# Kernel tuning notes

Hardware: AMD Instinct MI355X
Metric: run time of the kernel (lower is better)

The kernel has to match this reference:

```python
import jax, jax.numpy as jnp
import numpy as np

N, E, D = 50000, 200000, 128   # graph nodes, graph edges (= line-graph nodes), feature dim
L = 2                          # number of GINEConv iterations (linegraph init arg)


def _build_line_graph(col0, col1):
    """Exact sparse equivalent of torch.nonzero((col1[:,None]==col0[None,:]) & (col0[:,None]!=col1[:,None])).
    Returns line edges (i -> j) with col1[i] == col0[j] and edge i not a self-loop,
    plus edge_attr_idx = col1[lg_src] (the shared graph node)."""
    order = np.argsort(col0, kind='stable')              # edges grouped by source node
    counts = np.bincount(col0, minlength=N)              # out-degree per node
    offsets = np.concatenate([[0], np.cumsum(counts)[:-1]])
    lengths = np.where(col0 != col1, counts[col1], 0)    # successors of each non-self-loop edge
    M = int(lengths.sum())
    lg_src = np.repeat(np.arange(E), lengths)
    cum = np.cumsum(lengths)
    pos = np.arange(M) - np.repeat(cum - lengths, lengths)  # position within each successor block
    lg_dst = order[np.repeat(offsets[col1], lengths) + pos]
    edge_attr_idx = col1[lg_src]
    return lg_src.astype(np.int64), lg_dst.astype(np.int64), edge_attr_idx.astype(np.int64)


def setup_inputs() -> dict:
    rng = np.random.RandomState(0)
    col0 = rng.randint(0, N, size=E).astype(np.int64)
    col1 = rng.randint(0, N, size=E).astype(np.int64)
    lg_src, lg_dst, edge_attr_idx = _build_line_graph(col0, col1)

    key = jax.random.key(0)
    kx, k1, k2 = jax.random.split(key, 3)
    scale = (2.0 / D) ** 0.5
    return {
        'x':  jax.random.normal(kx, (N, D), dtype=jnp.float32),
        'W1': jax.random.normal(k1, (D, D), dtype=jnp.float32) * scale,
        'b1': jnp.zeros((D,), dtype=jnp.float32),
        'W2': jax.random.normal(k2, (D, D), dtype=jnp.float32) * scale,
        'b2': jnp.zeros((D,), dtype=jnp.float32),
        'col0': jnp.asarray(col0),
        'col1': jnp.asarray(col1),
        'lg_src': jnp.asarray(lg_src),
        'lg_dst': jnp.asarray(lg_dst),
        'edge_attr_idx': jnp.asarray(edge_attr_idx),
    }


def reference(x, W1, b1, W2, b2, col0, col1, lg_src, lg_dst, edge_attr_idx):
    # line-graph node features: mean of endpoint features of each original edge
    lgX = 0.5 * (x[col0] + x[col1])                       # [E, D]
    lgE = x[edge_attr_idx]                                # [M, D] line-edge attrs (fixed across iterations)

    for _ in range(L):  # GINEConv, eps = 0 (PyG default)
        m = jax.nn.relu(lgX[lg_src] + lgE)                # [M, D] messages
        aggr = jax.ops.segment_sum(m, lg_dst, num_segments=E)  # scatter-add at target line-nodes
        h = lgX + aggr                                    # (1 + eps) * x + aggr
        lgX = jax.nn.relu(h @ W1 + b1) @ W2 + b2          # gin_nn MLP

    # scatter_mean back to graph nodes by col1 (zeros where no incident edge, matching pad)
    sums = jax.ops.segment_sum(lgX, col1, num_segments=N)                     # [N, D]
    cnt = jax.ops.segment_sum(jnp.ones((lgX.shape[0], 1), lgX.dtype), col1, num_segments=N)
    gx = jnp.where(cnt > 0, sums / jnp.maximum(cnt, 1.0), 0.0)

    out = jax.nn.relu(gx)
    # dropout p=0.0 -> identity; residual=True
    return x + out
```

## Files before the change

kernel.cpp:

```cpp
#include <hip/hip_runtime.h>
#include <hip/hip_bf16.h>

constexpr int NN = 50000;
constexpr int EE = 200000;
typedef __bf16 bf16x8 __attribute__((ext_vector_type(8)));
typedef float f32x4 __attribute__((ext_vector_type(4)));

__device__ __forceinline__ float b2f(unsigned short s) {
    union { unsigned u; float f; } c; c.u = ((unsigned)s) << 16; return c.f;
}
__device__ __forceinline__ unsigned short bfbits(float f) {
    union { __bf16 b; unsigned short u; } c; c.b = (__bf16)f; return c.u;
}
__device__ __forceinline__ unsigned pkbf(float lo, float hi) {
    return ((unsigned)bfbits(hi) << 16) | bfbits(lo);
}
__device__ __forceinline__ unsigned short f2b(float f) {
    union { float f; unsigned u; } c; c.f = f;
    unsigned u = c.u + 0x7fffu + ((c.u >> 16) & 1u);
    return (unsigned short)(u >> 16);
}
__device__ __forceinline__ float xv(const void* p, long i, int f32m) {
    return f32m ? ((const float*)p)[i] : b2f(((const unsigned short*)p)[i]);
}
__device__ __forceinline__ int iv(const int* p, int i, int i64m) {
    return i64m ? p[2 * i] : p[i];
}

__global__ void k_detect(const unsigned short* x16, const int* c32, int* flg) {
    __shared__ int sf, si;
    int t = threadIdx.x;
    if (t == 0) { sf = 0; si = 1; }
    __syncthreads();
    for (int i = t; i < 16384; i += 256)
        if (((x16[i] >> 7) & 0xFF) == 0xFF) sf = 1;
    if (t < 64)
        if (c32[2 * t + 1] != 0) si = 0;
    __syncthreads();
    if (t == 0) { flg[0] = sf; flg[1] = si; }
}

__global__ void k_cast(const void* x, unsigned short* xb, const int* flg) {
    int i = blockIdx.x * 256 + threadIdx.x;
    if (i >= NN * 16) return;
    if (flg[0]) {
        const float4* xp = (const float4*)x + (size_t)i * 2;
        float4 u = xp[0], v = xp[1];
        uint4 o;
        o.x = pkbf(u.x, u.y); o.y = pkbf(u.z, u.w);
        o.z = pkbf(v.x, v.y); o.w = pkbf(v.z, v.w);
        ((uint4*)xb)[i] = o;
    } else {
        ((uint4*)xb)[i] = ((const uint4*)x)[i];
    }
}

__global__ void k_wfrag2(const void* W1, const void* W2,
                         unsigned short* Wf1, unsigned short* Wf2, const int* flg) {
    int f32m = flg[0];
    int g = blockIdx.x;
    const void* W = (g < 8) ? W1 : W2;
    unsigned short* Wf = (g < 8) ? Wf1 : Wf2;
    int chunk = (g & 7) * 256 + threadIdx.x;
    int l = chunk & 63, c = (chunk >> 6) & 3, t = chunk >> 8;
    int n = t * 16 + (l & 15), k0 = c * 32 + ((l >> 4) * 8);
    for (int j = 0; j < 8; j++) Wf[chunk * 8 + j] = bfbits(xv(W, (long)(k0 + j) * 128 + n, f32m));
}

__global__ void k_hist(const int* col1, int* counts, const int* flg) {
    int e = blockIdx.x * 256 + threadIdx.x;
    if (e >= EE) return;
    atomicAdd(&counts[iv(col1, e, flg[1])], 1);
}

__global__ void k_scan1(const int* counts, int* bsum) {
    __shared__ int sh[256];
    int b = blockIdx.x, t = threadIdx.x;
    int idx = b * 256 + t;
    sh[t] = (idx < NN) ? counts[idx] : 0;
    __syncthreads();
    for (int off = 128; off > 0; off >>= 1) {
        if (t < off) sh[t] += sh[t + off];
        __syncthreads();
    }
    if (t == 0) bsum[b] = sh[0];
}

__global__ void k_scan2(const int* counts, const int* bsum,
                        int* row_ptr, int* cursor) {
    __shared__ int sh[256];
    __shared__ int base_s;
    int b = blockIdx.x, t = threadIdx.x;
    sh[t] = (t < b) ? bsum[t] : 0;
    __syncthreads();
    for (int off = 128; off > 0; off >>= 1) {
        if (t < off) sh[t] += sh[t + off];
        __syncthreads();
    }
    if (t == 0) base_s = sh[0];
    __syncthreads();
    int idx = b * 256 + t;
    int v = (idx < NN) ? counts[idx] : 0;
    sh[t] = v;
    __syncthreads();
    for (int off = 1; off < 256; off <<= 1) {
        int add = (t >= off) ? sh[t - off] : 0;
        __syncthreads();
        sh[t] += add;
        __syncthreads();
    }
    int ex = base_s + sh[t] - v;
    if (idx < NN) { row_ptr[idx] = ex; cursor[idx] = ex; }
    if (idx == NN - 1) row_ptr[NN] = ex + v;
}

__global__ void k_cscatter(const int* col0, const int* col1, int* cursor,
                           unsigned* aux, int* node1, const int* flg) {
    int e = blockIdx.x * 256 + threadIdx.x;
    if (e >= EE) return;
    int i64m = flg[1];
    int a = iv(col0, e, i64m), b = iv(col1, e, i64m);
    int pos = atomicAdd(&cursor[b], 1);
    aux[pos] = (unsigned)a | (a == b ? 0x80000000u : 0u);
    node1[pos] = b;
}

__global__ void k_gath(const unsigned short* xb, const unsigned short* lgX,
                       const int* row_ptr, const unsigned* aux,
                       unsigned short* S, int mode) {
    int n = blockIdx.x * 4 + (threadIdx.x >> 6);
    if (n >= NN) return;
    int l = threadIdx.x & 63, k0 = l * 2;
    int lo = row_ptr[n], hi = row_ptr[n + 1];
    unsigned un = *(const unsigned*)(xb + (size_t)n * 128 + k0);
    float xn0 = b2f((unsigned short)un), xn1 = b2f((unsigned short)(un >> 16));
    float a0 = 0.0f, a1 = 0.0f;
    if (mode == 1) {
        for (int p = lo; p < hi; p++) {
            unsigned av = aux[p];
            if (av & 0x80000000u) continue;
            unsigned u = *(const unsigned*)(xb + (size_t)av * 128 + k0);
            a0 += fmaxf(0.5f * b2f((unsigned short)u) + 1.5f * xn0, 0.0f);
            a1 += fmaxf(0.5f * b2f((unsigned short)(u >> 16)) + 1.5f * xn1, 0.0f);
        }
    } else {
        for (int p = lo; p < hi; p++) {
            if (aux[p] & 0x80000000u) continue;
            unsigned u = *(const unsigned*)(lgX + (size_t)p * 128 + k0);
            a0 += fmaxf(b2f((unsigned short)u) + xn0, 0.0f);
            a1 += fmaxf(b2f((unsigned short)(u >> 16)) + xn1, 0.0f);
        }
    }
    *(unsigned*)(S + (size_t)n * 128 + k0) = pkbf(a0, a1);
}

__global__ __launch_bounds__(256, 8)
void k_fused(const unsigned short* A, const unsigned short* S,
             const unsigned* aux, const int* node1, const unsigned short* xb,
             const void* bias1, const void* bias2,
             const unsigned short* Wf1, const unsigned short* Wf2,
             unsigned short* Out, const int* flg, int initA) {
    __shared__ unsigned short Lds[8192];
    int f32m = flg[0];
    int tid = threadIdx.x;
    int w = tid >> 6, l = tid & 63;
    int lq = l >> 4, ln = l & 15;
    int e0 = blockIdx.x * 64 + w * 16;
    unsigned short* W_ = Lds + w * 2048;

    int row = e0 + ln;
    int aN = (int)(aux[row] & 0x7fffffffu);
    int bN = initA ? node1[row] : 0;
    bf16x8 af[4];
    for (int c = 0; c < 4; c++) {
        int k0 = c * 32 + lq * 8;
        uint4 svv = *(const uint4*)(S + (size_t)aN * 128 + k0);
        const unsigned short* sp = (const unsigned short*)&svv;
        if (initA) {
            uint4 xav = *(const uint4*)(xb + (size_t)aN * 128 + k0);
            uint4 xbv = *(const uint4*)(xb + (size_t)bN * 128 + k0);
            const unsigned short* xa = (const unsigned short*)&xav;
            const unsigned short* xc = (const unsigned short*)&xbv;
            for (int j = 0; j < 8; j++)
                af[c][j] = (__bf16)(0.5f * (b2f(xa[j]) + b2f(xc[j])) + b2f(sp[j]));
        } else {
            uint4 av = *(const uint4*)(A + (size_t)row * 128 + k0);
            const unsigned short* ap = (const unsigned short*)&av;
            for (int j = 0; j < 8; j++)
                af[c][j] = (__bf16)(b2f(ap[j]) + b2f(sp[j]));
        }
    }

    f32x4 acc[8];
    for (int j = 0; j < 8; j++)
        for (int r = 0; r < 4; r++) acc[j][r] = 0.0f;
    for (int c = 0; c < 4; c++) {
        for (int j = 0; j < 8; j++) {
            bf16x8 bf = *(const bf16x8*)(Wf1 + (size_t)(((j * 4 + c) * 64 + l) * 8));
            acc[j] = __builtin_amdgcn_mfma_f32_16x16x32_bf16(af[c], bf, acc[j], 0, 0, 0);
        }
    }

    for (int j = 0; j < 8; j++) {
        int n = j * 16 + ln;
        float bv = xv(bias1, n, f32m);
        int c2 = n >> 5, lhi = ((n >> 3) & 3) * 16, j2 = n & 7;
        for (int rg = 0; rg < 4; rg++) {
            float h = fmaxf(acc[j][rg] + bv, 0.0f);
            W_[(c2 * 64 + lhi + lq * 4 + rg) * 8 + j2] = bfbits(h);
        }
    }

    for (int j = 0; j < 8; j++)
        for (int r = 0; r < 4; r++) acc[j][r] = 0.0f;
    for (int c = 0; c < 4; c++) {
        bf16x8 a2 = *(const bf16x8*)(W_ + (c * 64 + l) * 8);
        for (int j = 0; j < 8; j++) {
            bf16x8 bf = *(const bf16x8*)(Wf2 + (size_t)(((j * 4 + c) * 64 + l) * 8));
            acc[j] = __builtin_amdgcn_mfma_f32_16x16x32_bf16(a2, bf, acc[j], 0, 0, 0);
        }
    }

    for (int j = 0; j < 8; j++) {
        int n = j * 16 + ln;
        float bv = xv(bias2, n, f32m);
        for (int rg = 0; rg < 4; rg++)
            W_[(lq * 4 + rg) * 128 + n] = bfbits(acc[j][rg] + bv);
    }
    for (int i = 0; i < 4; i++) {
        int idx = i * 64 + l;
        ((uint4*)Out)[(size_t)e0 * 16 + idx] = ((const uint4*)W_)[idx];
    }
}

__global__ void LGNNGINELayer_12463995093126_kernel(
    const void* x, const unsigned short* lgX, const int* row_ptr,
    void* out, const int* flg) {
    int n = blockIdx.x * 4 + (threadIdx.x >> 6);
    if (n >= NN) return;
    int l = threadIdx.x & 63, k0 = l * 2;
    int f32m = flg[0];
    int lo = row_ptr[n], hi = row_ptr[n + 1];
    float a0 = 0.0f, a1 = 0.0f;
    for (int p = lo; p < hi; p++) {
        unsigned u = *(const unsigned*)(lgX + (size_t)p * 128 + k0);
        a0 += b2f((unsigned short)u);
        a1 += b2f((unsigned short)(u >> 16));
    }
    float g0 = 0.0f, g1 = 0.0f;
    if (hi > lo) {
        float inv = 1.0f / (float)(hi - lo);
        g0 = fmaxf(a0 * inv, 0.0f);
        g1 = fmaxf(a1 * inv, 0.0f);
    }
    if (f32m) {
        ((float*)out)[(long)n * 128 + k0]     = ((const float*)x)[(long)n * 128 + k0] + g0;
        ((float*)out)[(long)n * 128 + k0 + 1] = ((const float*)x)[(long)n * 128 + k0 + 1] + g1;
    } else {
        unsigned u = *(const unsigned*)((const unsigned short*)x + (long)n * 128 + k0);
        float r0 = b2f((unsigned short)u) + g0;
        float r1 = b2f((unsigned short)(u >> 16)) + g1;
        *(unsigned*)((unsigned short*)out + (long)n * 128 + k0) = pkbf(r0, r1);
    }
}

extern "C" void kernel_launch(void* const* d_in, const int* in_sizes, int n_in,
                              void* d_out, int out_size, void* d_ws, size_t ws_size,
                              hipStream_t stream) {
    (void)in_sizes; (void)n_in; (void)out_size; (void)ws_size;
    const void* x = d_in[0];
    const void* W1 = d_in[1];
    const void* b1 = d_in[2];
    const void* W2 = d_in[3];
    const void* b2 = d_in[4];
    const int* col0 = (const int*)d_in[5];
    const int* col1 = (const int*)d_in[6];

    char* p = (char*)d_ws;
    unsigned short* lgX = (unsigned short*)p; p += (size_t)EE * 128 * 2;
    unsigned short* S = (unsigned short*)p;   p += (size_t)NN * 128 * 2;
    unsigned short* xb = (unsigned short*)p;  p += (size_t)NN * 128 * 2;
    int* row_ptr = (int*)p;                   p += (size_t)(NN + 16) * 4;
    int* cursor = (int*)p;                    p += (size_t)NN * 4;
    int* counts = (int*)p;                    p += (size_t)NN * 4;
    int* bsum = (int*)p;                      p += 256 * 4;
    unsigned* aux = (unsigned*)p;             p += (size_t)EE * 4;
    int* node1 = (int*)p;                     p += (size_t)EE * 4;
    int* flg = (int*)p;                       p += 256;
    unsigned short* Wf1 = (unsigned short*)p; p += 16384 * 2;
    unsigned short* Wf2 = (unsigned short*)p;

    int gB = EE / 64;
    int eB = (EE + 255) / 256;
    int nB4 = (NN + 3) / 4;
    int sB = (NN + 255) / 256;
    int cB = (NN * 16 + 255) / 256;

    k_detect<<<1, 256, 0, stream>>>((const unsigned short*)x, col0, flg);
    k_cast<<<cB, 256, 0, stream>>>(x, xb, flg);
    k_wfrag2<<<16, 256, 0, stream>>>(W1, W2, Wf1, Wf2, flg);

    hipMemsetAsync(counts, 0, (size_t)NN * 4, stream);
    k_hist<<<eB, 256, 0, stream>>>(col1, counts, flg);
    k_scan1<<<sB, 256, 0, stream>>>(counts, bsum);
    k_scan2<<<sB, 256, 0, stream>>>(counts, bsum, row_ptr, cursor);
    k_cscatter<<<eB, 256, 0, stream>>>(col0, col1, cursor, aux, node1, flg);

    k_gath<<<nB4, 256, 0, stream>>>(xb, lgX, row_ptr, aux, S, 1);
    k_fused<<<gB, 256, 0, stream>>>(lgX, S, aux, node1, xb, b1, b2,
                                    Wf1, Wf2, lgX, flg, 1);
    k_gath<<<nB4, 256, 0, stream>>>(xb, lgX, row_ptr, aux, S, 2);
    k_fused<<<gB, 256, 0, stream>>>(lgX, S, aux, node1, xb, b1, b2,
                                    Wf1, Wf2, lgX, flg, 0);
    LGNNGINELayer_12463995093126_kernel<<<nB4, 256, 0, stream>>>(
        x, lgX, row_ptr, d_out, flg);
}
```

Before: 385.2 us.

## Fuse final scatter-mean segment sums into second GIN MLP kernel epilogue

The second fused MLP kernel no longer writes its bf16 line-node features back to global memory. Instead it reduces its 64 sorted rows by destination node inside the block and writes fp32 partial sums into a node-sum buffer, using atomics only for segments that cross block boundaries. The final kernel becomes a simple elementwise divide-by-degree, relu and residual add. This removes the lgX write and re-read for the last layer, at the cost of an extra 25.6MB memset, fp32 atomics, and a serial 64-row loop run by one wave per block.

After: 400.0 us. +3.8%, slower.

```diff
diff --git a/kernel.cpp b/kernel.cpp
--- a/kernel.cpp
+++ b/kernel.cpp
@@ -14,11 +14,6 @@
 }
 __device__ __forceinline__ unsigned pkbf(float lo, float hi) {
     return ((unsigned)bfbits(hi) << 16) | bfbits(lo);
-}
-__device__ __forceinline__ unsigned short f2b(float f) {
-    union { float f; unsigned u; } c; c.f = f;
-    unsigned u = c.u + 0x7fffu + ((c.u >> 16) & 1u);
-    return (unsigned short)(u >> 16);
 }
 __device__ __forceinline__ float xv(const void* p, long i, int f32m) {
     return f32m ? ((const float*)p)[i] : b2f(((const unsigned short*)p)[i]);
@@ -159,24 +154,26 @@
              const unsigned* aux, const int* node1, const unsigned short* xb,
              const void* bias1, const void* bias2,
              const unsigned short* Wf1, const unsigned short* Wf2,
-             unsigned short* Out, const int* flg, int initA) {
+             unsigned short* Out, float* NS, const int* flg, int mode) {
     __shared__ unsigned short Lds[8192];
+    __shared__ int nd[66];
     int f32m = flg[0];
     int tid = threadIdx.x;
     int w = tid >> 6, l = tid & 63;
     int lq = l >> 4, ln = l & 15;
-    int e0 = blockIdx.x * 64 + w * 16;
+    int eb = blockIdx.x * 64;
+    int e0 = eb + w * 16;
     unsigned short* W_ = Lds + w * 2048;
 
     int row = e0 + ln;
     int aN = (int)(aux[row] & 0x7fffffffu);
-    int bN = initA ? node1[row] : 0;
+    int bN = (mode == 1) ? node1[row] : 0;
     bf16x8 af[4];
     for (int c = 0; c < 4; c++) {
         int k0 = c * 32 + lq * 8;
         uint4 svv = *(const uint4*)(S + (size_t)aN * 128 + k0);
         const unsigned short* sp = (const unsigned short*)&svv;
-        if (initA) {
+        if (mode == 1) {
             uint4 xav = *(const uint4*)(xb + (size_t)aN * 128 + k0);
             uint4 xbv = *(const uint4*)(xb + (size_t)bN * 128 + k0);
             const unsigned short* xa = (const unsigned short*)&xav;
@@ -227,41 +224,55 @@
         for (int rg = 0; rg < 4; rg++)
             W_[(lq * 4 + rg) * 128 + n] = bfbits(acc[j][rg] + bv);
     }
-    for (int i = 0; i < 4; i++) {
-        int idx = i * 64 + l;
-        ((uint4*)Out)[(size_t)e0 * 16 + idx] = ((const uint4*)W_)[idx];
+
+    if (mode == 1) {
+        for (int i = 0; i < 4; i++) {
+            int idx = i * 64 + l;
+            ((uint4*)Out)[(size_t)e0 * 16 + idx] = ((const uint4*)W_)[idx];
+        }
+        return;
+    }
+
+    if (tid < 64) nd[tid] = node1[eb + tid];
+    else if (tid == 64) nd[64] = (eb > 0) ? node1[eb - 1] : -1;
+    else if (tid == 65) nd[65] = (eb + 64 < EE) ? node1[eb + 64] : -1;
+    __syncthreads();
+    if (tid < 64) {
+        int c2 = tid * 2;
+        float a0 = 0.0f, a1 = 0.0f;
+        int cur = nd[0];
+        bool openL = (nd[64] == cur);
+        for (int r = 0; r < 64; r++) {
+            unsigned v = *(const unsigned*)(Lds + ((r >> 4) * 2048 + (r & 15) * 128 + c2));
+            a0 += b2f((unsigned short)v);
+            a1 += b2f((unsigned short)(v >> 16));
+            bool last = (r == 63);
+            int nxt = last ? nd[65] : nd[r + 1];
+            if (nxt != cur || last) {
+                bool closedR = (nxt != cur);
+                float* dst = NS + (size_t)cur * 128 + c2;
+                if (!openL && closedR) { dst[0] = a0; dst[1] = a1; }
+                else { atomicAdd(&dst[0], a0); atomicAdd(&dst[1], a1); }
+                a0 = 0.0f; a1 = 0.0f;
+                cur = nxt;
+                openL = false;
+            }
+        }
     }
 }
 
 __global__ void LGNNGINELayer_12463995093126_kernel(
-    const void* x, const unsigned short* lgX, const int* row_ptr,
+    const void* x, const float* NS, const int* row_ptr,
     void* out, const int* flg) {
-    int n = blockIdx.x * 4 + (threadIdx.x >> 6);
-    if (n >= NN) return;
-    int l = threadIdx.x & 63, k0 = l * 2;
-    int f32m = flg[0];
-    int lo = row_ptr[n], hi = row_ptr[n + 1];
-    float a0 = 0.0f, a1 = 0.0f;
-    for (int p = lo; p < hi; p++) {
-        unsigned u = *(const unsigned*)(lgX + (size_t)p * 128 + k0);
-        a0 += b2f((unsigned short)u);
-        a1 += b2f((unsigned short)(u >> 16));
-    }
-    float g0 = 0.0f, g1 = 0.0f;
-    if (hi > lo) {
-        float inv = 1.0f / (float)(hi - lo);
-        g0 = fmaxf(a0 * inv, 0.0f);
-        g1 = fmaxf(a1 * inv, 0.0f);
-    }
-    if (f32m) {
-        ((float*)out)[(long)n * 128 + k0]     = ((const float*)x)[(long)n * 128 + k0] + g0;
-        ((float*)out)[(long)n * 128 + k0 + 1] = ((const float*)x)[(long)n * 128 + k0 + 1] + g1;
-    } else {
-        unsigned u = *(const unsigned*)((const unsigned short*)x + (long)n * 128 + k0);
-        float r0 = b2f((unsigned short)u) + g0;
-        float r1 = b2f((unsigned short)(u >> 16)) + g1;
-        *(unsigned*)((unsigned short*)out + (long)n * 128 + k0) = pkbf(r0, r1);
-    }
+    int i = blockIdx.x * 256 + threadIdx.x;
+    if (i >= NN * 128) return;
+    int n = i >> 7;
+    int deg = row_ptr[n + 1] - row_ptr[n];
+    float g = 0.0f;
+    if (deg > 0) g = fmaxf(NS[i] / (float)deg, 0.0f);
+    float r = xv(x, i, flg[0]) + g;
+    if (flg[0]) ((float*)out)[i] = r;
+    else ((unsigned short*)out)[i] = bfbits(r);
 }
 
 extern "C" void kernel_launch(void* const* d_in, const int* in_sizes, int n_in,
@@ -280,6 +291,7 @@
     unsigned short* lgX = (unsigned short*)p; p += (size_t)EE * 128 * 2;
     unsigned short* S = (unsigned short*)p;   p += (size_t)NN * 128 * 2;
     unsigned short* xb = (unsigned short*)p;  p += (size_t)NN * 128 * 2;
+    float* NS = (float*)p;                    p += (size_t)NN * 128 * 4;
     int* row_ptr = (int*)p;                   p += (size_t)(NN + 16) * 4;
     int* cursor = (int*)p;                    p += (size_t)NN * 4;
     int* counts = (int*)p;                    p += (size_t)NN * 4;
@@ -293,6 +305,7 @@
     int gB = EE / 64;
     int eB = (EE + 255) / 256;
     int nB4 = (NN + 3) / 4;
+    int nBe = (NN * 128) / 256;
     int sB = (NN + 255) / 256;
     int cB = (NN * 16 + 255) / 256;
 
@@ -308,10 +321,11 @@
 
     k_gath<<<nB4, 256, 0, stream>>>(xb, lgX, row_ptr, aux, S, 1);
     k_fused<<<gB, 256, 0, stream>>>(lgX, S, aux, node1, xb, b1, b2,
-                                    Wf1, Wf2, lgX, flg, 1);
+                                    Wf1, Wf2, lgX, NS, flg, 1);
     k_gath<<<nB4, 256, 0, stream>>>(xb, lgX, row_ptr, aux, S, 2);
+    hipMemsetAsync(NS, 0, (size_t)NN * 128 * 4, stream);
     k_fused<<<gB, 256, 0, stream>>>(lgX, S, aux, node1, xb, b1, b2,
-                                    Wf1, Wf2, lgX, flg, 0);
-    LGNNGINELayer_12463995093126_kernel<<<nB4, 256, 0, stream>>>(
-        x, lgX, row_ptr, d_out, flg);
-}
+                                    Wf1, Wf2, lgX, NS, flg, 2);
+    LGNNGINELayer_12463995093126_kernel<<<nBe, 256, 0, stream>>>(
+        x, NS, row_ptr, d_out, flg);
+}
```

## Keep line-graph features in two orderings to make fused gathers coalesced

Applied to the files above, without the earlier changes.

Builds a second CSR ordering by col0 next to the col1 ordering. The fused MLP kernel now processes edges in col0 order, so the node-level sums T are gathered per source node. Results are written both sequentially (col0 copy, used as the residual input) and scattered into col1 order for the gather and final kernels. The initial lgX term is folded into the node sum in k_gath, which drops the x[col0] read in the first MLP. Setup kernels are merged and counts are doubled to cover both orderings. The cost is an extra E×D output buffer with scattered 16-byte row writes, plus extra atomics and index arrays.

Measured after the change: 395.2 us. 2.6% more time.

```diff
diff --git a/kernel.cpp b/kernel.cpp
--- a/kernel.cpp
+++ b/kernel.cpp
@@ -3,6 +3,8 @@
 
 constexpr int NN = 50000;
 constexpr int EE = 200000;
+constexpr int SB = (NN + 255) / 256;
+constexpr int CB = (NN * 16 + 255) / 256;
 typedef __bf16 bf16x8 __attribute__((ext_vector_type(8)));
 typedef float f32x4 __attribute__((ext_vector_type(4)));
 
@@ -14,11 +16,6 @@
 }
 __device__ __forceinline__ unsigned pkbf(float lo, float hi) {
     return ((unsigned)bfbits(hi) << 16) | bfbits(lo);
-}
-__device__ __forceinline__ unsigned short f2b(float f) {
-    union { float f; unsigned u; } c; c.f = f;
-    unsigned u = c.u + 0x7fffu + ((c.u >> 16) & 1u);
-    return (unsigned short)(u >> 16);
 }
 __device__ __forceinline__ float xv(const void* p, long i, int f32m) {
     return f32m ? ((const float*)p)[i] : b2f(((const unsigned short*)p)[i]);
@@ -40,44 +37,50 @@
     if (t == 0) { flg[0] = sf; flg[1] = si; }
 }
 
-__global__ void k_cast(const void* x, unsigned short* xb, const int* flg) {
-    int i = blockIdx.x * 256 + threadIdx.x;
-    if (i >= NN * 16) return;
-    if (flg[0]) {
-        const float4* xp = (const float4*)x + (size_t)i * 2;
-        float4 u = xp[0], v = xp[1];
-        uint4 o;
-        o.x = pkbf(u.x, u.y); o.y = pkbf(u.z, u.w);
-        o.z = pkbf(v.x, v.y); o.w = pkbf(v.z, v.w);
-        ((uint4*)xb)[i] = o;
+__global__ void k_prep(const void* x, unsigned short* xb,
+                       const void* W1, const void* W2,
+                       unsigned short* Wf1, unsigned short* Wf2, const int* flg) {
+    int g = blockIdx.x, f32m = flg[0];
+    if (g < CB) {
+        int i = g * 256 + threadIdx.x;
+        if (i >= NN * 16) return;
+        if (f32m) {
+            const float4* xp = (const float4*)x + (size_t)i * 2;
+            float4 u = xp[0], v = xp[1];
+            uint4 o;
+            o.x = pkbf(u.x, u.y); o.y = pkbf(u.z, u.w);
+            o.z = pkbf(v.x, v.y); o.w = pkbf(v.z, v.w);
+            ((uint4*)xb)[i] = o;
+        } else {
+            ((uint4*)xb)[i] = ((const uint4*)x)[i];
+        }
     } else {
-        ((uint4*)xb)[i] = ((const uint4*)x)[i];
-    }
-}
-
-__global__ void k_wfrag2(const void* W1, const void* W2,
-                         unsigned short* Wf1, unsigned short* Wf2, const int* flg) {
-    int f32m = flg[0];
-    int g = blockIdx.x;
-    const void* W = (g < 8) ? W1 : W2;
-    unsigned short* Wf = (g < 8) ? Wf1 : Wf2;
-    int chunk = (g & 7) * 256 + threadIdx.x;
-    int l = chunk & 63, c = (chunk >> 6) & 3, t = chunk >> 8;
-    int n = t * 16 + (l & 15), k0 = c * 32 + ((l >> 4) * 8);
-    for (int j = 0; j < 8; j++) Wf[chunk * 8 + j] = bfbits(xv(W, (long)(k0 + j) * 128 + n, f32m));
-}
-
-__global__ void k_hist(const int* col1, int* counts, const int* flg) {
+        int gg = g - CB;
+        const void* W = (gg < 8) ? W1 : W2;
+        unsigned short* Wf = (gg < 8) ? Wf1 : Wf2;
+        int chunk = (gg & 7) * 256 + threadIdx.x;
+        int l = chunk & 63, c = (chunk >> 6) & 3, t = chunk >> 8;
+        int n = t * 16 + (l & 15), k0 = c * 32 + ((l >> 4) * 8);
+        for (int j = 0; j < 8; j++)
+            Wf[chunk * 8 + j] = bfbits(xv(W, (long)(k0 + j) * 128 + n, f32m));
+    }
+}
+
+__global__ void k_hist2(const int* col0, const int* col1, int* counts, const int* flg) {
     int e = blockIdx.x * 256 + threadIdx.x;
     if (e >= EE) return;
-    atomicAdd(&counts[iv(col1, e, flg[1])], 1);
+    int i64m = flg[1];
+    atomicAdd(&counts[iv(col1, e, i64m)], 1);
+    atomicAdd(&counts[NN + iv(col0, e, i64m)], 1);
 }
 
 __global__ void k_scan1(const int* counts, int* bsum) {
     __shared__ int sh[256];
     int b = blockIdx.x, t = threadIdx.x;
-    int idx = b * 256 + t;
-    sh[t] = (idx < NN) ? counts[idx] : 0;
+    int aid = (b >= SB) ? 1 : 0;
+    int b2 = b - aid * SB;
+    int idx = b2 * 256 + t;
+    sh[t] = (idx < NN) ? counts[aid * NN + idx] : 0;
     __syncthreads();
     for (int off = 128; off > 0; off >>= 1) {
         if (t < off) sh[t] += sh[t + off];
@@ -87,11 +90,13 @@
 }
 
 __global__ void k_scan2(const int* counts, const int* bsum,
-                        int* row_ptr, int* cursor) {
+                        int* row_ptr, int* cursor1, int* cursor0) {
     __shared__ int sh[256];
     __shared__ int base_s;
     int b = blockIdx.x, t = threadIdx.x;
-    sh[t] = (t < b) ? bsum[t] : 0;
+    int aid = (b >= SB) ? 1 : 0;
+    int b2 = b - aid * SB;
+    sh[t] = (t < b2) ? bsum[aid * SB + t] : 0;
     __syncthreads();
     for (int off = 128; off > 0; off >>= 1) {
         if (t < off) sh[t] += sh[t + off];
@@ -99,8 +104,8 @@
     }
     if (t == 0) base_s = sh[0];
     __syncthreads();
-    int idx = b * 256 + t;
-    int v = (idx < NN) ? counts[idx] : 0;
+    int idx = b2 * 256 + t;
+    int v = (idx < NN) ? counts[aid * NN + idx] : 0;
     sh[t] = v;
     __syncthreads();
     for (int off = 1; off < 256; off <<= 1) {
@@ -110,19 +115,24 @@
         __syncthreads();
     }
     int ex = base_s + sh[t] - v;
-    if (idx < NN) { row_ptr[idx] = ex; cursor[idx] = ex; }
-    if (idx == NN - 1) row_ptr[NN] = ex + v;
-}
-
-__global__ void k_cscatter(const int* col0, const int* col1, int* cursor,
-                           unsigned* aux, int* node1, const int* flg) {
+    if (idx < NN) {
+        if (aid == 0) { row_ptr[idx] = ex; cursor1[idx] = ex; }
+        else cursor0[idx] = ex;
+    }
+    if (aid == 0 && idx == NN - 1) row_ptr[NN] = ex + v;
+}
+
+__global__ void k_cscatter2(const int* col0, const int* col1,
+                            int* cursor1, int* cursor0,
+                            unsigned* aux, int* a0, int* b0, int* p0, const int* flg) {
     int e = blockIdx.x * 256 + threadIdx.x;
     if (e >= EE) return;
     int i64m = flg[1];
     int a = iv(col0, e, i64m), b = iv(col1, e, i64m);
-    int pos = atomicAdd(&cursor[b], 1);
-    aux[pos] = (unsigned)a | (a == b ? 0x80000000u : 0u);
-    node1[pos] = b;
+    int p1 = atomicAdd(&cursor1[b], 1);
+    aux[p1] = (unsigned)a | (a == b ? 0x80000000u : 0u);
+    int q = atomicAdd(&cursor0[a], 1);
+    a0[q] = a; b0[q] = b; p0[q] = p1;
 }
 
 __global__ void k_gath(const unsigned short* xb, const unsigned short* lgX,
@@ -134,32 +144,33 @@
     int lo = row_ptr[n], hi = row_ptr[n + 1];
     unsigned un = *(const unsigned*)(xb + (size_t)n * 128 + k0);
     float xn0 = b2f((unsigned short)un), xn1 = b2f((unsigned short)(un >> 16));
-    float a0 = 0.0f, a1 = 0.0f;
+    float a0_ = 0.0f, a1_ = 0.0f;
     if (mode == 1) {
         for (int p = lo; p < hi; p++) {
             unsigned av = aux[p];
             if (av & 0x80000000u) continue;
             unsigned u = *(const unsigned*)(xb + (size_t)av * 128 + k0);
-            a0 += fmaxf(0.5f * b2f((unsigned short)u) + 1.5f * xn0, 0.0f);
-            a1 += fmaxf(0.5f * b2f((unsigned short)(u >> 16)) + 1.5f * xn1, 0.0f);
-        }
+            a0_ += fmaxf(0.5f * b2f((unsigned short)u) + 1.5f * xn0, 0.0f);
+            a1_ += fmaxf(0.5f * b2f((unsigned short)(u >> 16)) + 1.5f * xn1, 0.0f);
+        }
+        a0_ += 0.5f * xn0; a1_ += 0.5f * xn1;
     } else {
         for (int p = lo; p < hi; p++) {
             if (aux[p] & 0x80000000u) continue;
             unsigned u = *(const unsigned*)(lgX + (size_t)p * 128 + k0);
-            a0 += fmaxf(b2f((unsigned short)u) + xn0, 0.0f);
-            a1 += fmaxf(b2f((unsigned short)(u >> 16)) + xn1, 0.0f);
-        }
-    }
-    *(unsigned*)(S + (size_t)n * 128 + k0) = pkbf(a0, a1);
+            a0_ += fmaxf(b2f((unsigned short)u) + xn0, 0.0f);
+            a1_ += fmaxf(b2f((unsigned short)(u >> 16)) + xn1, 0.0f);
+        }
+    }
+    *(unsigned*)(S + (size_t)n * 128 + k0) = pkbf(a0_, a1_);
 }
 
 __global__ __launch_bounds__(256, 8)
-void k_fused(const unsigned short* A, const unsigned short* S,
-             const unsigned* aux, const int* node1, const unsigned short* xb,
+void k_fused(const unsigned short* TS, const unsigned short* Aseq,
+             const unsigned short* xb, const int* a0, const int* b0, const int* p0,
              const void* bias1, const void* bias2,
              const unsigned short* Wf1, const unsigned short* Wf2,
-             unsigned short* Out, const int* flg, int initA) {
+             unsigned short* Oc0, unsigned short* Oc1, const int* flg, int mode) {
     __shared__ unsigned short Lds[8192];
     int f32m = flg[0];
     int tid = threadIdx.x;
@@ -168,26 +179,24 @@
     int e0 = blockIdx.x * 64 + w * 16;
     unsigned short* W_ = Lds + w * 2048;
 
-    int row = e0 + ln;
-    int aN = (int)(aux[row] & 0x7fffffffu);
-    int bN = initA ? node1[row] : 0;
+    int q = e0 + ln;
+    int aN = a0[q];
+    int bN = (mode == 1) ? b0[q] : 0;
     bf16x8 af[4];
     for (int c = 0; c < 4; c++) {
         int k0 = c * 32 + lq * 8;
-        uint4 svv = *(const uint4*)(S + (size_t)aN * 128 + k0);
-        const unsigned short* sp = (const unsigned short*)&svv;
-        if (initA) {
-            uint4 xav = *(const uint4*)(xb + (size_t)aN * 128 + k0);
+        uint4 tvv = *(const uint4*)(TS + (size_t)aN * 128 + k0);
+        const unsigned short* tp = (const unsigned short*)&tvv;
+        if (mode == 1) {
             uint4 xbv = *(const uint4*)(xb + (size_t)bN * 128 + k0);
-            const unsigned short* xa = (const unsigned short*)&xav;
             const unsigned short* xc = (const unsigned short*)&xbv;
             for (int j = 0; j < 8; j++)
-                af[c][j] = (__bf16)(0.5f * (b2f(xa[j]) + b2f(xc[j])) + b2f(sp[j]));
+                af[c][j] = (__bf16)(b2f(tp[j]) + 0.5f * b2f(xc[j]));
         } else {
-            uint4 av = *(const uint4*)(A + (size_t)row * 128 + k0);
+            uint4 av = *(const uint4*)(Aseq + (size_t)q * 128 + k0);
             const unsigned short* ap = (const unsigned short*)&av;
             for (int j = 0; j < 8; j++)
-                af[c][j] = (__bf16)(b2f(ap[j]) + b2f(sp[j]));
+                af[c][j] = (__bf16)(b2f(ap[j]) + b2f(tp[j]));
         }
     }
 
@@ -227,9 +236,18 @@
         for (int rg = 0; rg < 4; rg++)
             W_[(lq * 4 + rg) * 128 + n] = bfbits(acc[j][rg] + bv);
     }
+
+    if (mode == 1) {
+        for (int i = 0; i < 4; i++) {
+            int idx = i * 64 + l;
+            ((uint4*)Oc0)[(size_t)e0 * 16 + idx] = ((const uint4*)W_)[idx];
+        }
+    }
     for (int i = 0; i < 4; i++) {
         int idx = i * 64 + l;
-        ((uint4*)Out)[(size_t)e0 * 16 + idx] = ((const uint4*)W_)[idx];
+        int r = idx >> 4;
+        int tgt = p0[e0 + r];
+        ((uint4*)Oc1)[(size_t)tgt * 16 + (idx & 15)] = ((const uint4*)W_)[idx];
     }
 }
 
@@ -241,17 +259,17 @@
     int l = threadIdx.x & 63, k0 = l * 2;
     int f32m = flg[0];
     int lo = row_ptr[n], hi = row_ptr[n + 1];
-    float a0 = 0.0f, a1 = 0.0f;
+    float a0_ = 0.0f, a1_ = 0.0f;
     for (int p = lo; p < hi; p++) {
         unsigned u = *(const unsigned*)(lgX + (size_t)p * 128 + k0);
-        a0 += b2f((unsigned short)u);
-        a1 += b2f((unsigned short)(u >> 16));
+        a0_ += b2f((unsigned short)u);
+        a1_ += b2f((unsigned short)(u >> 16));
     }
     float g0 = 0.0f, g1 = 0.0f;
     if (hi > lo) {
         float inv = 1.0f / (float)(hi - lo);
-        g0 = fmaxf(a0 * inv, 0.0f);
-        g1 = fmaxf(a1 * inv, 0.0f);
+        g0 = fmaxf(a0_ * inv, 0.0f);
+        g1 = fmaxf(a1_ * inv, 0.0f);
     }
     if (f32m) {
         ((float*)out)[(long)n * 128 + k0]     = ((const float*)x)[(long)n * 128 + k0] + g0;
@@ -277,41 +295,43 @@
     const int* col1 = (const int*)d_in[6];
 
     char* p = (char*)d_ws;
-    unsigned short* lgX = (unsigned short*)p; p += (size_t)EE * 128 * 2;
-    unsigned short* S = (unsigned short*)p;   p += (size_t)NN * 128 * 2;
-    unsigned short* xb = (unsigned short*)p;  p += (size_t)NN * 128 * 2;
-    int* row_ptr = (int*)p;                   p += (size_t)(NN + 16) * 4;
-    int* cursor = (int*)p;                    p += (size_t)NN * 4;
-    int* counts = (int*)p;                    p += (size_t)NN * 4;
-    int* bsum = (int*)p;                      p += 256 * 4;
-    unsigned* aux = (unsigned*)p;             p += (size_t)EE * 4;
-    int* node1 = (int*)p;                     p += (size_t)EE * 4;
-    int* flg = (int*)p;                       p += 256;
-    unsigned short* Wf1 = (unsigned short*)p; p += 16384 * 2;
+    unsigned short* lgXc0 = (unsigned short*)p; p += (size_t)EE * 128 * 2;
+    unsigned short* lgXc1 = (unsigned short*)p; p += (size_t)EE * 128 * 2;
+    unsigned short* T = (unsigned short*)p;     p += (size_t)NN * 128 * 2;
+    unsigned short* xb = (unsigned short*)p;    p += (size_t)NN * 128 * 2;
+    int* row_ptr = (int*)p;                     p += (size_t)(NN + 16) * 4;
+    int* cursor1 = (int*)p;                     p += (size_t)NN * 4;
+    int* cursor0 = (int*)p;                     p += (size_t)NN * 4;
+    int* counts = (int*)p;                      p += (size_t)2 * NN * 4;
+    int* bsum = (int*)p;                        p += 512 * 4;
+    unsigned* aux = (unsigned*)p;               p += (size_t)EE * 4;
+    int* a0 = (int*)p;                          p += (size_t)EE * 4;
+    int* b0 = (int*)p;                          p += (size_t)EE * 4;
+    int* p0 = (int*)p;                          p += (size_t)EE * 4;
+    int* flg = (int*)p;                         p += 256;
+    unsigned short* Wf1 = (unsigned short*)p;   p += 16384 * 2;
     unsigned short* Wf2 = (unsigned short*)p;
 
     int gB = EE / 64;
     int eB = (EE + 255) / 256;
     int nB4 = (NN + 3) / 4;
-    int sB = (NN + 255) / 256;
-    int cB = (NN * 16 + 255) / 256;
 
     k_detect<<<1, 256, 0, stream>>>((const unsigned short*)x, col0, flg);
-    k_cast<<<cB, 256, 0, stream>>>(x, xb, flg);
-    k_wfrag2<<<16, 256, 0, stream>>>(W1, W2, Wf1, Wf2, flg);
-
-    hipMemsetAsync(counts, 0, (size_t)NN * 4, stream);
-    k_hist<<<eB, 256, 0, stream>>>(col1, counts, flg);
-    k_scan1<<<sB, 256, 0, stream>>>(counts, bsum);
-    k_scan2<<<sB, 256, 0, stream>>>(counts, bsum, row_ptr, cursor);
-    k_cscatter<<<eB, 256, 0, stream>>>(col0, col1, cursor, aux, node1, flg);
-
-    k_gath<<<nB4, 256, 0, stream>>>(xb, lgX, row_ptr, aux, S, 1);
-    k_fused<<<gB, 256, 0, stream>>>(lgX, S, aux, node1, xb, b1, b2,
-                                    Wf1, Wf2, lgX, flg, 1);
-    k_gath<<<nB4, 256, 0, stream>>>(xb, lgX, row_ptr, aux, S, 2);
-    k_fused<<<gB, 256, 0, stream>>>(lgX, S, aux, node1, xb, b1, b2,
-                                    Wf1, Wf2, lgX, flg, 0);
+    k_prep<<<CB + 16, 256, 0, stream>>>(x, xb, W1, W2, Wf1, Wf2, flg);
+
+    hipMemsetAsync(counts, 0, (size_t)2 * NN * 4, stream);
+    k_hist2<<<eB, 256, 0, stream>>>(col0, col1, counts, flg);
+    k_scan1<<<2 * SB, 256, 0, stream>>>(counts, bsum);
+    k_scan2<<<2 * SB, 256, 0, stream>>>(counts, bsum, row_ptr, cursor1, cursor0);
+    k_cscatter2<<<eB, 256, 0, stream>>>(col0, col1, cursor1, cursor0,
+                                        aux, a0, b0, p0, flg);
+
+    k_gath<<<nB4, 256, 0, stream>>>(xb, lgXc1, row_ptr, aux, T, 1);
+    k_fused<<<gB, 256, 0, stream>>>(T, lgXc0, xb, a0, b0, p0, b1, b2,
+                                    Wf1, Wf2, lgXc0, lgXc1, flg, 1);
+    k_gath<<<nB4, 256, 0, stream>>>(xb, lgXc1, row_ptr, aux, T, 2);
+    k_fused<<<gB, 256, 0, stream>>>(T, lgXc0, xb, a0, b0, p0, b1, b2,
+                                    Wf1, Wf2, lgXc0, lgXc1, flg, 2);
     LGNNGINELayer_12463995093126_kernel<<<nB4, 256, 0, stream>>>(
-        x, lgX, row_ptr, d_out, flg);
-}
+        x, lgXc1, row_ptr, d_out, flg);
+}
```
